# Kernel tuning notes

Measured on AMD Instinct MI355X. Metric: run time of the kernel, lower is better.

The kernel has to match this reference:

```python
import jax, jax.numpy as jnp
import numpy as np

N = 50000
E = 800000
F_IN = 500
ID_DIM = 128
HID = 128
N_CLS = 40


def _init_linear(key, fan_in, fan_out, bias=True):
    k1, k2 = jax.random.split(key)
    bound = 1.0 / np.sqrt(fan_in)
    W = jax.random.uniform(k1, (fan_in, fan_out), minval=-bound, maxval=bound, dtype=jnp.float32)
    if bias:
        b = jax.random.uniform(k2, (fan_out,), minval=-bound, maxval=bound, dtype=jnp.float32)
        return W, b
    return W, None


def setup_inputs() -> dict:
    key = jax.random.key(0)
    ks = jax.random.split(key, 10)
    x = jax.random.normal(ks[0], (N, F_IN), dtype=jnp.float32)
    edge_index = jax.random.randint(ks[1], (2, E), 0, N, dtype=jnp.int32)
    W_map, b_map = _init_linear(ks[2], F_IN, ID_DIM)
    Wl1, bl1 = _init_linear(ks[3], ID_DIM, HID)
    Wr1, _ = _init_linear(ks[4], ID_DIM, HID, bias=False)
    Wl2, bl2 = _init_linear(ks[5], HID, 2 * HID)
    Wr2, _ = _init_linear(ks[6], HID, 2 * HID, bias=False)
    Wl3, bl3 = _init_linear(ks[7], 2 * HID, N_CLS)
    Wr3, _ = _init_linear(ks[8], 2 * HID, N_CLS, bias=False)
    return {"x": x, "edge_index": edge_index,
            "W_map": W_map, "b_map": b_map,
            "Wl1": Wl1, "bl1": bl1, "Wr1": Wr1,
            "Wl2": Wl2, "bl2": bl2, "Wr2": Wr2,
            "Wl3": Wl3, "bl3": bl3, "Wr3": Wr3}


def _sage_conv(x, src, dst, Wl, bl, Wr):
    # mean aggregation of source features into destination nodes
    agg = jax.ops.segment_sum(x[src], dst, num_segments=N)  # [N, d]
    cnt = jax.ops.segment_sum(jnp.ones((src.shape[0],), x.dtype), dst, num_segments=N)
    mean = agg / jnp.maximum(cnt, 1.0)[:, None]
    # SAGEConv (normalize=False): lin_l(mean_neigh) + lin_r(x), bias only on lin_l
    return mean @ Wl + bl + x @ Wr


def reference(x, edge_index, W_map, b_map, Wl1, bl1, Wr1, Wl2, bl2, Wr2, Wl3, bl3, Wr3):
    src, dst = edge_index[0], edge_index[1]
    h = x @ W_map + b_map                      # [N, 128]
    h = jax.nn.relu(_sage_conv(h, src, dst, Wl1, bl1, Wr1))   # dropout is identity in eval
    h = jax.nn.relu(_sage_conv(h, src, dst, Wl2, bl2, Wr2))
    h = _sage_conv(h, src, dst, Wl3, bl3, Wr3)
    return jax.nn.log_softmax(h, axis=1)
```

## Files before the change

### kernel.cpp

```cpp
#include <hip/hip_runtime.h>
#include <math.h>

#define NN 50000
#define NE 800000
#define FIN 500
#define NCLS 40
#define NB 196

typedef short short8 __attribute__((ext_vector_type(8)));
typedef float f32x4 __attribute__((ext_vector_type(4)));

__device__ __forceinline__ unsigned short f2bf(float f) {
    unsigned u = __float_as_uint(f);
    unsigned r = (u + 0x7FFFu + ((u >> 16) & 1u)) >> 16;
    return (unsigned short)r;
}
__device__ __forceinline__ float bf2f(unsigned short h) {
    return __uint_as_float(((unsigned)h) << 16);
}

typedef const __attribute__((address_space(1))) void gv1;
typedef __attribute__((address_space(3))) void lv3;
__device__ __forceinline__ void gl16(const void* g, void* l) {
    __builtin_amdgcn_global_load_lds((gv1*)g, (lv3*)l, 16, 0, 0);
}

__global__ void k_wsplit(const float* __restrict__ W, short* __restrict__ dst,
                         int Ksrc, int Ncols, int Kpad, int BN, int koff,
                         int noff, int llog) {
    int i = blockIdx.x * 256 + threadIdx.x;
    int len = 1 << llog;
    if (i >= Ncols * len) return;
    int n = i >> llog, kk = i & (len - 1);
    float v = (kk < Ksrc) ? W[(size_t)kk * Ncols + n] : 0.f;
    unsigned short hi = f2bf(v);
    float lo = v - bf2f(hi);
    int nd = noff + n, kd = koff + kk;
    int yb = nd / BN, r = nd % BN;
    int ck = kd >> 6, kin = kd & 63;
    int c16h = (kin >> 3) ^ (r & 7);
    size_t rowb = (((size_t)yb * (Kpad >> 6) + ck) * BN + r) * 128;
    dst[rowb + c16h * 8 + (kin & 7)] = (short)hi;
    dst[rowb + (8 + c16h) * 8 + (kin & 7)] = (short)f2bf(lo);
}

__global__ void k_count(const int* __restrict__ dst, int* __restrict__ deg) {
    int e = blockIdx.x * blockDim.x + threadIdx.x;
    if (e < NE) atomicAdd(&deg[dst[e]], 1);
}

__global__ void k_scan1(const int* __restrict__ deg, int* __restrict__ offs,
                        int* __restrict__ bsum) {
    __shared__ int sm[256];
    int tid = threadIdx.x;
    int i = blockIdx.x * 256 + tid;
    int v = (i < NN) ? deg[i] : 0;
    sm[tid] = v;
    __syncthreads();
    for (int off = 1; off < 256; off <<= 1) {
        int t = (tid >= off) ? sm[tid - off] : 0;
        __syncthreads();
        sm[tid] += t;
        __syncthreads();
    }
    if (i < NN) offs[i] = sm[tid] - v;
    if (tid == 255) bsum[blockIdx.x] = sm[255];
}

__global__ void k_scan2(const int* __restrict__ bsum, int* __restrict__ bpre,
                        int* __restrict__ offs) {
    __shared__ int sm[256];
    int tid = threadIdx.x;
    int v = (tid < NB) ? bsum[tid] : 0;
    sm[tid] = v;
    __syncthreads();
    for (int off = 1; off < 256; off <<= 1) {
        int t = (tid >= off) ? sm[tid - off] : 0;
        __syncthreads();
        sm[tid] += t;
        __syncthreads();
    }
    if (tid < NB) bpre[tid] = sm[tid] - v;
    if (tid == 255) offs[NN] = sm[255];
}

__global__ void k_scan3(int* __restrict__ offs, const int* __restrict__ bpre,
                        int* __restrict__ cursor) {
    int i = blockIdx.x * 256 + threadIdx.x;
    if (i < NN) {
        int v = offs[i] + bpre[blockIdx.x];
        offs[i] = v;
        cursor[i] = v;
    }
}

__global__ void k_scatter(const int* __restrict__ src, const int* __restrict__ dst,
                          int* __restrict__ cursor, int* __restrict__ ssrc) {
    int e = blockIdx.x * blockDim.x + threadIdx.x;
    if (e < NE) {
        int p = atomicAdd(&cursor[dst[e]], 1);
        ssrc[p] = src[e];
    }
}

__global__ __launch_bounds__(256) void k_aggb(
    const short* __restrict__ hb, const int* __restrict__ offs,
    const int* __restrict__ ssrc, short* __restrict__ mH) {
    int wid = (blockIdx.x * 256 + threadIdx.x) >> 6;
    int lane = threadIdx.x & 63;
    if (wid >= NN) return;
    int sub = lane >> 4, l16 = lane & 15;
    int beg = offs[wid], end = offs[wid + 1];
    f32x4 a0 = {0.f, 0.f, 0.f, 0.f}, a1 = {0.f, 0.f, 0.f, 0.f};
    for (int i = beg + sub; i < end; i += 16) {
        int i1 = i + 4, i2 = i + 8, i3 = i + 12;
        int em1 = end - 1;
        int s0 = ssrc[i];
        int s1 = ssrc[min(i1, em1)];
        int s2 = ssrc[min(i2, em1)];
        int s3 = ssrc[min(i3, em1)];
        float w1 = (i1 < end) ? 1.f : 0.f;
        float w2 = (i2 < end) ? 1.f : 0.f;
        float w3 = (i3 < end) ? 1.f : 0.f;
        short8 v0 = *(const short8*)(hb + (size_t)s0 * 128 + l16 * 8);
        short8 v1 = *(const short8*)(hb + (size_t)s1 * 128 + l16 * 8);
        short8 v2 = *(const short8*)(hb + (size_t)s2 * 128 + l16 * 8);
        short8 v3 = *(const short8*)(hb + (size_t)s3 * 128 + l16 * 8);
#pragma unroll
        for (int j = 0; j < 4; ++j) {
            a0[j] += (bf2f((unsigned short)v0[j]) + w1 * bf2f((unsigned short)v1[j])) +
                     (w2 * bf2f((unsigned short)v2[j]) + w3 * bf2f((unsigned short)v3[j]));
            a1[j] += (bf2f((unsigned short)v0[j + 4]) + w1 * bf2f((unsigned short)v1[j + 4])) +
                     (w2 * bf2f((unsigned short)v2[j + 4]) + w3 * bf2f((unsigned short)v3[j + 4]));
        }
    }
#pragma unroll
    for (int j = 0; j < 4; ++j) {
        a0[j] += __shfl_xor(a0[j], 16);
        a0[j] += __shfl_xor(a0[j], 32);
        a1[j] += __shfl_xor(a1[j], 16);
        a1[j] += __shfl_xor(a1[j], 32);
    }
    if (sub == 0) {
        float inv = 1.f / fmaxf((float)(end - beg), 1.f);
        a0 *= inv; a1 *= inv;
        short8 hv;
#pragma unroll
        for (int j = 0; j < 4; ++j) {
            hv[j] = (short)f2bf(a0[j]);
            hv[j + 4] = (short)f2bf(a1[j]);
        }
        *(short8*)(mH + (size_t)wid * 128 + l16 * 8) = hv;
    }
}

template <int BN, int KPAD, int KS0, int KREAL, bool AFP32, bool RELU, bool PQ>
__global__ __launch_bounds__(512, 4) void k_mm8(
    const void* __restrict__ A0v, const short* __restrict__ A1,
    const short* __restrict__ Bg, const float* __restrict__ bias,
    short* __restrict__ CH, int ldc,
    float* __restrict__ F0, float* __restrict__ F1, int splitN,
    int M, int N) {
    constexpr int NT = BN / 16;
    constexpr int C = KPAD / 64;
    constexpr int PT = (BN * 16) / 512;
    constexpr int SLAB = BN * 128;
    constexpr int NA = AFP32 ? 4 : 0;
    static_assert((BN * 16) % 512 == 0, "staging divisibility");
    static_assert(C >= 3, "peel structure needs >=3 chunks");
    __shared__ short Bs[2 * SLAB];
    int tid = threadIdx.x;
    int wave = tid >> 6, lane = tid & 63;
    int quad = lane >> 4, l16 = lane & 15;
    int colBase = blockIdx.y * BN;
    int r0 = blockIdx.x * 128 + wave * 16 + l16;
    int r0c = min(r0, M - 1);
    const short* Bbase = Bg + (size_t)blockIdx.y * (C * SLAB);

    f32x4 acc[NT];
#pragma unroll
    for (int n = 0; n < NT; ++n) acc[n] = (f32x4){0.f, 0.f, 0.f, 0.f};

    auto stageB = [&](int buf, int ck) {
        const short* src = Bbase + (size_t)ck * SLAB;
        short* db = Bs + buf * SLAB;
#pragma unroll
        for (int u = 0; u < PT; ++u) {
            int base = u * 512 + wave * 64;
            gl16(src + (size_t)(base + lane) * 8, db + (size_t)base * 8);
        }
    };

    short8 aPre[AFP32 ? 2 : (2 * C)];
    short8 aCur[2];
    f32x4 fN[2][4];
    const float* Af = (const float*)A0v + (size_t)r0c * (size_t)KREAL;

    auto ldA32 = [&](int slot, int ck) {
#pragma unroll
        for (int s = 0; s < 2; ++s) {
            int kg = ck * 64 + s * 32 + quad * 8;
            f32x4 f0 = {0.f, 0.f, 0.f, 0.f}, f1 = {0.f, 0.f, 0.f, 0.f};
            if (kg < KREAL) f0 = *(const f32x4*)(Af + kg);
            if (kg + 4 < KREAL) f1 = *(const f32x4*)(Af + kg + 4);
            fN[slot][s * 2] = f0;
            fN[slot][s * 2 + 1] = f1;
        }
    };
    auto cvtA = [&](int slot) {
#pragma unroll
        for (int s = 0; s < 2; ++s) {
            short8 a;
#pragma unroll
            for (int j = 0; j < 4; ++j) {
                a[j] = (short)f2bf(fN[slot][s * 2][j]);
                a[j + 4] = (short)f2bf(fN[slot][s * 2 + 1][j]);
            }
            aCur[s] = a;
        }
    };
    auto compute = [&](int ck) {
        const short* bb = Bs + (ck & 1) * SLAB;
#pragma unroll
        for (int s = 0; s < 2; ++s) {
            short8 a;
            if constexpr (AFP32) a = aCur[s];
            else                 a = aPre[ck * 2 + s];
#pragma unroll
            for (int n = 0; n < NT; ++n) {
                int r = n * 16 + l16;
                int ch = (s * 4 + quad) ^ (r & 7);
                short8 bh = *(const short8*)(bb + r * 128 + ch * 8);
                short8 bl = *(const short8*)(bb + r * 128 + (8 + ch) * 8);
                acc[n] = __builtin_amdgcn_mfma_f32_16x16x32_bf16(a, bh, acc[n], 0, 0, 0);
                acc[n] = __builtin_amdgcn_mfma_f32_16x16x32_bf16(a, bl, acc[n], 0, 0, 0);
            }
        }
    };

    if constexpr (!AFP32) {
        const short* A0 = (const short*)A0v;
#pragma unroll
        for (int c = 0; c < C; ++c) {
            const bool seg = (c * 64 >= KS0);
            const short* ap = seg ? A1 : A0;
            const int w = seg ? (KPAD - KS0) : KS0;
            const int col = c * 64 - (seg ? KS0 : 0);
#pragma unroll
            for (int s = 0; s < 2; ++s)
                aPre[c * 2 + s] =
                    *(const short8*)(ap + (size_t)r0c * w + col + s * 32 + quad * 8);
        }
    }
    stageB(0, 0);
    if constexpr (AFP32) { ldA32(0, 0); ldA32(1, 1); }

#pragma unroll
    for (int ck = 0; ck <= C - 2; ++ck) {
        asm volatile("s_waitcnt vmcnt(%0)" ::"n"(NA) : "memory");
        __builtin_amdgcn_s_barrier();
        __builtin_amdgcn_sched_barrier(0);
        stageB((ck + 1) & 1, ck + 1);
        if constexpr (AFP32) {
            cvtA(ck & 1);
            if (ck + 2 < C) ldA32(ck & 1, ck + 2);
        }
        compute(ck);
    }
    {
        asm volatile("s_waitcnt vmcnt(0)" ::: "memory");
        __builtin_amdgcn_s_barrier();
        __builtin_amdgcn_sched_barrier(0);
        if constexpr (AFP32) cvtA((C - 1) & 1);
        compute(C - 1);
    }

    int gr0 = blockIdx.x * 128 + wave * 16 + quad * 4;
#pragma unroll
    for (int n = 0; n < NT; ++n) {
        int gc = colBase + n * 16 + l16;
        if (gc >= N) continue;
        float b = bias ? bias[gc] : 0.f;
#pragma unroll
        for (int r = 0; r < 4; ++r) {
            int gr = gr0 + r;
            if (gr < M) {
                float v = acc[n][r] + b;
                if (RELU) v = fmaxf(v, 0.f);
                if constexpr (PQ) {
                    if (gc < splitN) CH[(size_t)gr * ldc + gc] = (short)f2bf(v);
                    else             F0[(size_t)gr * (N - splitN) + (gc - splitN)] = v;
                } else {
                    if (CH) CH[(size_t)gr * ldc + gc] = (short)f2bf(v);
                    if (F0) {
                        if (gc < splitN) F0[(size_t)gr * splitN + gc] = v;
                        else             F1[(size_t)gr * (N - splitN) + (gc - splitN)] = v;
                    }
                }
            }
        }
    }
}

__global__ __launch_bounds__(256) void k_final(
    const short* __restrict__ pH, const float* __restrict__ q,
    const int* __restrict__ offs, const int* __restrict__ ssrc,
    const float* __restrict__ bl3, float* __restrict__ out) {
    int wid = (blockIdx.x * 256 + threadIdx.x) >> 6;
    int lane = threadIdx.x & 63;
    if (wid >= NN) return;
    bool act = lane < NCLS;
    int beg = offs[wid], end = offs[wid + 1];
    float a0 = 0.f, a1 = 0.f, a2 = 0.f, a3 = 0.f;
    for (int i = beg; i < end; i += 4) {
        int em1 = end - 1;
        int s0 = ssrc[i];
        int s1 = ssrc[min(i + 1, em1)];
        int s2 = ssrc[min(i + 2, em1)];
        int s3 = ssrc[min(i + 3, em1)];
        float w1 = (i + 1 < end) ? 1.f : 0.f;
        float w2 = (i + 2 < end) ? 1.f : 0.f;
        float w3 = (i + 3 < end) ? 1.f : 0.f;
        if (act) {
            a0 += bf2f((unsigned short)pH[(size_t)s0 * 64 + lane]);
            a1 += w1 * bf2f((unsigned short)pH[(size_t)s1 * 64 + lane]);
            a2 += w2 * bf2f((unsigned short)pH[(size_t)s2 * 64 + lane]);
            a3 += w3 * bf2f((unsigned short)pH[(size_t)s3 * 64 + lane]);
        }
    }
    float inv = 1.f / fmaxf((float)(end - beg), 1.f);
    float v = act ? ((a0 + a1) + (a2 + a3)) * inv + bl3[lane] + q[(size_t)wid * NCLS + lane]
                  : -INFINITY;
    float m = v;
#pragma unroll
    for (int off = 32; off > 0; off >>= 1) m = fmaxf(m, __shfl_xor(m, off));
    float e = act ? expf(v - m) : 0.f;
    float s = e;
#pragma unroll
    for (int off = 32; off > 0; off >>= 1) s += __shfl_xor(s, off);
    float ls = logf(s);
    if (act) out[(size_t)wid * NCLS + lane] = v - m - ls;
}

extern "C" void kernel_launch(void* const* d_in, const int* in_sizes, int n_in,
                              void* d_out, int out_size, void* d_ws, size_t ws_size,
                              hipStream_t stream) {
    const float* x    = (const float*)d_in[0];
    const int*   ei   = (const int*)d_in[1];
    const int*   esrc = ei;
    const int*   edst = ei + NE;
    const float* W_map = (const float*)d_in[2];
    const float* b_map = (const float*)d_in[3];
    const float* Wl1   = (const float*)d_in[4];
    const float* bl1   = (const float*)d_in[5];
    const float* Wr1   = (const float*)d_in[6];
    const float* Wl2   = (const float*)d_in[7];
    const float* bl2   = (const float*)d_in[8];
    const float* Wr2   = (const float*)d_in[9];
    const float* Wl3   = (const float*)d_in[10];
    const float* bl3   = (const float*)d_in[11];
    const float* Wr3   = (const float*)d_in[12];
    float* out = (float*)d_out;

    char* ws = (char*)d_ws;
    short* h0H = (short*)ws; ws += (size_t)NN * 128 * 2;
    short* m0H = (short*)ws; ws += (size_t)NN * 128 * 2;
    short* h1H = (short*)ws; ws += (size_t)NN * 128 * 2;
    short* m1H = (short*)ws; ws += (size_t)NN * 128 * 2;
    short* h2H = (short*)ws; ws += (size_t)NN * 256 * 2;
    short* pH  = (short*)ws; ws += (size_t)NN * 64 * 2;
    float* q   = (float*)ws; ws += (size_t)NN * NCLS * 4;
    short* wt  = (short*)ws; ws += (size_t)376832 * 2;
    int* deg    = (int*)ws;  ws += (size_t)NN * 4;
    int* offs   = (int*)ws;  ws += (size_t)(NN + 2) * 4;
    int* cursor = (int*)ws;  ws += (size_t)NN * 4;
    int* ssrc   = (int*)ws;  ws += (size_t)NE * 4;
    int* bsum   = (int*)ws;  ws += (size_t)256 * 4;
    int* bpre   = (int*)ws;  ws += (size_t)256 * 4;

    short* m_w  = wt + 0;
    short* b1w  = wt + 131072;
    short* b2w  = wt + 196608;
    short* b3w  = wt + 327680;

    (void)hipMemsetAsync(b3w, 0, (size_t)49152 * 2, stream);
    k_wsplit<<<(128 * 512 + 255) / 256, 256, 0, stream>>>(W_map, m_w, FIN, 128, 512, 128, 0, 0, 9);
    k_wsplit<<<(128 * 128 + 255) / 256, 256, 0, stream>>>(Wr1, b1w, 128, 128, 256, 128, 0, 0, 7);
    k_wsplit<<<(128 * 128 + 255) / 256, 256, 0, stream>>>(Wl1, b1w, 128, 128, 256, 128, 128, 0, 7);
    k_wsplit<<<(256 * 128 + 255) / 256, 256, 0, stream>>>(Wr2, b2w, 128, 256, 256, 128, 0, 0, 7);
    k_wsplit<<<(256 * 128 + 255) / 256, 256, 0, stream>>>(Wl2, b2w, 128, 256, 256, 128, 128, 0, 7);
    k_wsplit<<<(40 * 256 + 255) / 256, 256, 0, stream>>>(Wl3, b3w, 256, 40, 256, 96, 0, 0, 8);
    k_wsplit<<<(40 * 256 + 255) / 256, 256, 0, stream>>>(Wr3, b3w, 256, 40, 256, 96, 0, 40, 8);

    (void)hipMemsetAsync(deg, 0, (size_t)NN * 4, stream);
    k_count<<<(NE + 255) / 256, 256, 0, stream>>>(edst, deg);
    k_scan1<<<NB, 256, 0, stream>>>(deg, offs, bsum);
    k_scan2<<<1, 256, 0, stream>>>(bsum, bpre, offs);
    k_scan3<<<NB, 256, 0, stream>>>(offs, bpre, cursor);
    k_scatter<<<(NE + 255) / 256, 256, 0, stream>>>(esrc, edst, cursor, ssrc);

    const int g128 = (NN + 127) / 128;
    const int aggBlocks = (NN * 64) / 256;

    k_mm8<128, 512, 512, FIN, true, false, false><<<dim3(g128, 1), 512, 0, stream>>>(
        (const void*)x, nullptr, m_w, b_map,
        h0H, 128, nullptr, nullptr, 0, NN, 128);

    k_aggb<<<aggBlocks, 256, 0, stream>>>(h0H, offs, ssrc, m0H);

    k_mm8<128, 256, 128, 256, false, true, false><<<dim3(g128, 1), 512, 0, stream>>>(
        (const void*)h0H, m0H, b1w, bl1,
        h1H, 128, nullptr, nullptr, 0, NN, 128);

    k_aggb<<<aggBlocks, 256, 0, stream>>>(h1H, offs, ssrc, m1H);

    k_mm8<128, 256, 128, 256, false, true, false><<<dim3(g128, 2), 512, 0, stream>>>(
        (const void*)h1H, m1H, b2w, bl2,
        h2H, 256, nullptr, nullptr, 0, NN, 256);

    k_mm8<96, 256, 256, 256, false, false, true><<<dim3(g128, 1), 512, 0, stream>>>(
        (const void*)h2H, nullptr, b3w, nullptr,
        pH, 64, q, nullptr, NCLS, NN, 80);

    k_final<<<aggBlocks, 256, 0, stream>>>(pH, q, offs, ssrc, bl3, out);
}
```

Baseline: 451.6 us.

## Fuse degree count with weight split, and edge scatter with input GEMM

Merges the degree-counting atomics, all seven weight-split launches and the b3w zero-fill into one heterogeneous launch. It also fuses the CSR scatter with the first feature-mapping GEMM in a second launch, partitioned by block index. This cuts launch count and lets the independent scatter work overlap with the large GEMM. The trade-off is that scatter blocks now run under the GEMM's launch bounds and LDS allocation, which may limit their occupancy. The memset of b3w is replaced by explicit zeroing of only the padding rows.

Measured after the change: 413.1 us. 8.5% less time.

```diff
diff --git a/kernel.cpp b/kernel.cpp
--- a/kernel.cpp
+++ b/kernel.cpp
@@ -6,6 +6,9 @@
 #define FIN 500
 #define NCLS 40
 #define NB 196
+#define G0 391
+#define CNTB 1563
+#define WSE 192512
 
 typedef short short8 __attribute__((ext_vector_type(8)));
 typedef float f32x4 __attribute__((ext_vector_type(4)));
@@ -25,13 +28,10 @@
     __builtin_amdgcn_global_load_lds((gv1*)g, (lv3*)l, 16, 0, 0);
 }
 
-__global__ void k_wsplit(const float* __restrict__ W, short* __restrict__ dst,
-                         int Ksrc, int Ncols, int Kpad, int BN, int koff,
-                         int noff, int llog) {
-    int i = blockIdx.x * 256 + threadIdx.x;
-    int len = 1 << llog;
-    if (i >= Ncols * len) return;
-    int n = i >> llog, kk = i & (len - 1);
+__device__ __forceinline__ void wsplit_one(
+    const float* __restrict__ W, short* __restrict__ dst,
+    int Ksrc, int Ncols, int Kpad, int BN, int koff, int noff, int llog, int i) {
+    int n = i >> llog, kk = i & ((1 << llog) - 1);
     float v = (kk < Ksrc) ? W[(size_t)kk * Ncols + n] : 0.f;
     unsigned short hi = f2bf(v);
     float lo = v - bf2f(hi);
@@ -44,9 +44,34 @@
     dst[rowb + (8 + c16h) * 8 + (kin & 7)] = (short)f2bf(lo);
 }
 
-__global__ void k_count(const int* __restrict__ dst, int* __restrict__ deg) {
-    int e = blockIdx.x * blockDim.x + threadIdx.x;
-    if (e < NE) atomicAdd(&deg[dst[e]], 1);
+__global__ __launch_bounds__(512) void k_mega1(
+    const int* __restrict__ edst, int* __restrict__ deg,
+    const float* __restrict__ W_map,
+    const float* __restrict__ Wr1, const float* __restrict__ Wl1,
+    const float* __restrict__ Wr2, const float* __restrict__ Wl2,
+    const float* __restrict__ Wl3, const float* __restrict__ Wr3,
+    short* __restrict__ m_w, short* __restrict__ b1w,
+    short* __restrict__ b2w, short* __restrict__ b3w) {
+    int tid = threadIdx.x;
+    if (blockIdx.x < CNTB) {
+        int e = blockIdx.x * 512 + tid;
+        if (e < NE) atomicAdd(&deg[edst[e]], 1);
+        return;
+    }
+    int idx = (blockIdx.x - CNTB) * 512 + tid;
+    if (idx < 65536)       wsplit_one(W_map, m_w, FIN, 128, 512, 128, 0, 0, 9, idx);
+    else if (idx < 81920)  wsplit_one(Wr1, b1w, 128, 128, 256, 128, 0, 0, 7, idx - 65536);
+    else if (idx < 98304)  wsplit_one(Wl1, b1w, 128, 128, 256, 128, 128, 0, 7, idx - 81920);
+    else if (idx < 131072) wsplit_one(Wr2, b2w, 128, 256, 256, 128, 0, 0, 7, idx - 98304);
+    else if (idx < 163840) wsplit_one(Wl2, b2w, 128, 256, 256, 128, 128, 0, 7, idx - 131072);
+    else if (idx < 174080) wsplit_one(Wl3, b3w, 256, 40, 256, 96, 0, 0, 8, idx - 163840);
+    else if (idx < 184320) wsplit_one(Wr3, b3w, 256, 40, 256, 96, 0, 40, 8, idx - 174080);
+    else if (idx < WSE) {
+        int j = idx - 184320;
+        int ck = j >> 11, rem = j & 2047;
+        int r = 80 + (rem >> 7), c = rem & 127;
+        b3w[((size_t)(ck * 96 + r)) * 128 + c] = 0;
+    }
 }
 
 __global__ void k_scan1(const int* __restrict__ deg, int* __restrict__ offs,
@@ -91,15 +116,6 @@
         int v = offs[i] + bpre[blockIdx.x];
         offs[i] = v;
         cursor[i] = v;
-    }
-}
-
-__global__ void k_scatter(const int* __restrict__ src, const int* __restrict__ dst,
-                          int* __restrict__ cursor, int* __restrict__ ssrc) {
-    int e = blockIdx.x * blockDim.x + threadIdx.x;
-    if (e < NE) {
-        int p = atomicAdd(&cursor[dst[e]], 1);
-        ssrc[p] = src[e];
     }
 }
 
@@ -155,12 +171,12 @@
 }
 
 template <int BN, int KPAD, int KS0, int KREAL, bool AFP32, bool RELU, bool PQ>
-__global__ __launch_bounds__(512, 4) void k_mm8(
+__device__ __forceinline__ void gemm_body(
     const void* __restrict__ A0v, const short* __restrict__ A1,
     const short* __restrict__ Bg, const float* __restrict__ bias,
     short* __restrict__ CH, int ldc,
     float* __restrict__ F0, float* __restrict__ F1, int splitN,
-    int M, int N) {
+    int M, int N, int bx, int by) {
     constexpr int NT = BN / 16;
     constexpr int C = KPAD / 64;
     constexpr int PT = (BN * 16) / 512;
@@ -172,10 +188,10 @@
     int tid = threadIdx.x;
     int wave = tid >> 6, lane = tid & 63;
     int quad = lane >> 4, l16 = lane & 15;
-    int colBase = blockIdx.y * BN;
-    int r0 = blockIdx.x * 128 + wave * 16 + l16;
+    int colBase = by * BN;
+    int r0 = bx * 128 + wave * 16 + l16;
     int r0c = min(r0, M - 1);
-    const short* Bbase = Bg + (size_t)blockIdx.y * (C * SLAB);
+    const short* Bbase = Bg + (size_t)by * (C * SLAB);
 
     f32x4 acc[NT];
 #pragma unroll
@@ -275,7 +291,7 @@
         compute(C - 1);
     }
 
-    int gr0 = blockIdx.x * 128 + wave * 16 + quad * 4;
+    int gr0 = bx * 128 + wave * 16 + quad * 4;
 #pragma unroll
     for (int n = 0; n < NT; ++n) {
         int gc = colBase + n * 16 + l16;
@@ -298,6 +314,35 @@
                     }
                 }
             }
+        }
+    }
+}
+
+template <int BN, int KPAD, int KS0, int KREAL, bool AFP32, bool RELU, bool PQ>
+__global__ __launch_bounds__(512, 4) void k_mm8(
+    const void* __restrict__ A0v, const short* __restrict__ A1,
+    const short* __restrict__ Bg, const float* __restrict__ bias,
+    short* __restrict__ CH, int ldc,
+    float* __restrict__ F0, float* __restrict__ F1, int splitN,
+    int M, int N) {
+    gemm_body<BN, KPAD, KS0, KREAL, AFP32, RELU, PQ>(
+        A0v, A1, Bg, bias, CH, ldc, F0, F1, splitN, M, N, blockIdx.x, blockIdx.y);
+}
+
+__global__ __launch_bounds__(512, 4) void k_mega2(
+    const float* __restrict__ x, const short* __restrict__ m_w,
+    const float* __restrict__ b_map, short* __restrict__ h0H,
+    const int* __restrict__ esrc, const int* __restrict__ edst,
+    int* __restrict__ cursor, int* __restrict__ ssrc) {
+    if (blockIdx.x < G0) {
+        gemm_body<128, 512, 512, FIN, true, false, false>(
+            (const void*)x, nullptr, m_w, b_map,
+            h0H, 128, nullptr, nullptr, 0, NN, 128, blockIdx.x, 0);
+    } else {
+        int e = (blockIdx.x - G0) * 512 + threadIdx.x;
+        if (e < NE) {
+            int p = atomicAdd(&cursor[edst[e]], 1);
+            ssrc[p] = esrc[e];
         }
     }
 }
@@ -383,28 +428,19 @@
     short* b2w  = wt + 196608;
     short* b3w  = wt + 327680;
 
-    (void)hipMemsetAsync(b3w, 0, (size_t)49152 * 2, stream);
-    k_wsplit<<<(128 * 512 + 255) / 256, 256, 0, stream>>>(W_map, m_w, FIN, 128, 512, 128, 0, 0, 9);
-    k_wsplit<<<(128 * 128 + 255) / 256, 256, 0, stream>>>(Wr1, b1w, 128, 128, 256, 128, 0, 0, 7);
-    k_wsplit<<<(128 * 128 + 255) / 256, 256, 0, stream>>>(Wl1, b1w, 128, 128, 256, 128, 128, 0, 7);
-    k_wsplit<<<(256 * 128 + 255) / 256, 256, 0, stream>>>(Wr2, b2w, 128, 256, 256, 128, 0, 0, 7);
-    k_wsplit<<<(256 * 128 + 255) / 256, 256, 0, stream>>>(Wl2, b2w, 128, 256, 256, 128, 128, 0, 7);
-    k_wsplit<<<(40 * 256 + 255) / 256, 256, 0, stream>>>(Wl3, b3w, 256, 40, 256, 96, 0, 0, 8);
-    k_wsplit<<<(40 * 256 + 255) / 256, 256, 0, stream>>>(Wr3, b3w, 256, 40, 256, 96, 0, 40, 8);
+    const int g128 = (NN + 127) / 128;
+    const int aggBlocks = (NN * 64) / 256;
+    const int wsb = (WSE + 511) / 512;
 
     (void)hipMemsetAsync(deg, 0, (size_t)NN * 4, stream);
-    k_count<<<(NE + 255) / 256, 256, 0, stream>>>(edst, deg);
+    k_mega1<<<CNTB + wsb, 512, 0, stream>>>(edst, deg, W_map, Wr1, Wl1, Wr2, Wl2,
+                                            Wl3, Wr3, m_w, b1w, b2w, b3w);
+
     k_scan1<<<NB, 256, 0, stream>>>(deg, offs, bsum);
     k_scan2<<<1, 256, 0, stream>>>(bsum, bpre, offs);
     k_scan3<<<NB, 256, 0, stream>>>(offs, bpre, cursor);
-    k_scatter<<<(NE + 255) / 256, 256, 0, stream>>>(esrc, edst, cursor, ssrc);
-
-    const int g128 = (NN + 127) / 128;
-    const int aggBlocks = (NN * 64) / 256;
-
-    k_mm8<128, 512, 512, FIN, true, false, false><<<dim3(g128, 1), 512, 0, stream>>>(
-        (const void*)x, nullptr, m_w, b_map,
-        h0H, 128, nullptr, nullptr, 0, NN, 128);
+
+    k_mega2<<<G0 + CNTB, 512, 0, stream>>>(x, m_w, b_map, h0H, esrc, edst, cursor, ssrc);
 
     k_aggb<<<aggBlocks, 256, 0, stream>>>(h0H, offs, ssrc, m0H);
 
```
